# Kernel tuning notes

Hardware: AMD Instinct MI355X
Metric: run time of the kernel (lower is better)

## Reference

```python
import jax, jax.numpy as jnp
import numpy as np

M = 16           # size_graph_filter (nodes per hidden prototype graph)
S = 16           # size_subgraph
D_IN = 128       # input_dim
H = 64           # hidden_dim
O = 32           # out_dim (number of hidden prototype graphs)
B = 32768        # batch of subgraphs
MAX_STEP = 3
BN_EPS = 1e-5


def setup_inputs() -> dict:
    key = jax.random.key(0)
    ks = jax.random.split(key, 8)
    adj = jax.random.uniform(ks[0], (B, S, S), dtype=jnp.float32)
    adj = 0.5 * (adj + jnp.swapaxes(adj, 1, 2))  # symmetric weighted adjacency
    features = jax.random.normal(ks[1], (B, S, D_IN), dtype=jnp.float32)
    # learned parameters (per torch init: uniform inits, Linear default-like fc_in)
    W_in = jax.random.normal(ks[2], (D_IN, H), dtype=jnp.float32) * (1.0 / np.sqrt(D_IN))
    b_in = jnp.zeros((H,), dtype=jnp.float32)
    features_hidden = jax.random.uniform(ks[3], (M, H, O), dtype=jnp.float32)          # U(0,1)
    adj_hidden = jax.random.uniform(ks[4], (M * (M - 1) // 2, O), dtype=jnp.float32,
                                    minval=-1.0, maxval=1.0)                            # U(-1,1)
    bn_gamma = jnp.ones((O,), dtype=jnp.float32)
    bn_beta = jnp.zeros((O,), dtype=jnp.float32)
    return {"adj": adj, "features": features, "W_in": W_in, "b_in": b_in,
            "features_hidden": features_hidden, "adj_hidden": adj_hidden,
            "bn_gamma": bn_gamma, "bn_beta": bn_beta}


def reference(adj, features, W_in, b_in, features_hidden, adj_hidden, bn_gamma, bn_beta):
    # Build symmetric hidden adjacency (M, M, O) from triu-packed parameters.
    iu, ju = jnp.triu_indices(M, k=1)
    A = jnp.zeros((M, M, O), dtype=adj_hidden.dtype)
    A = A.at[iu, ju, :].set(jax.nn.relu(adj_hidden))
    A = A + jnp.swapaxes(A, 0, 1)

    x = jax.nn.sigmoid(features @ W_in + b_in)   # (B, S, H)
    z = features_hidden                           # (M, H, O)

    acc = jnp.zeros((B, O), dtype=x.dtype)
    for step in range(MAX_STEP):
        if step > 0:
            x = jnp.einsum('bst,bth->bsh', adj, x)        # propagate on input subgraphs
            z = jnp.einsum('mpo,pho->mho', A, z)          # propagate on hidden graphs
        # random-walk kernel value between each subgraph and each prototype
        t = jnp.einsum('mho,bsh->bo', z, x)               # sum over prototype & subgraph nodes
        acc = acc + t
    out = acc / MAX_STEP

    # BatchNorm1d (training-mode batch statistics), then sigmoid; dropout p used in eval = identity
    mean = jnp.mean(out, axis=0)
    var = jnp.var(out, axis=0)
    out = (out - mean) / jnp.sqrt(var + BN_EPS) * bn_gamma + bn_beta
    return jax.nn.sigmoid(out)
```

## Files before the change

### kernel.cpp

```cpp
#include <hip/hip_runtime.h>


typedef short  vec8s  __attribute__((ext_vector_type(8)));
typedef short  vec4s  __attribute__((ext_vector_type(4)));
typedef float  f32x4  __attribute__((ext_vector_type(4)));
typedef unsigned short vec4us __attribute__((ext_vector_type(4)));

#define NB      32768
#define SS      16
#define DIN     128
#define HH      64
#define OO      32
#define MM      16

__device__ __forceinline__ float bf2f(unsigned short u) {
    return __uint_as_float(((unsigned int)u) << 16);
}
__device__ __forceinline__ unsigned short f2bf(float f) {
    unsigned int u = __float_as_uint(f);
    unsigned int r = (u + 0x7fffu + ((u >> 16) & 1u)) >> 16;
    return (unsigned short)r;
}
template<bool F32>
__device__ __forceinline__ float ldv(const void* p, int i) {
    if (F32) return ((const float*)p)[i];
    return bf2f(((const unsigned short*)p)[i]);
}
__device__ __forceinline__ vec8s pack8(f32x4 lo, f32x4 hi) {
    union { unsigned int u[4]; vec8s v; } r;
    unsigned int a0 = __float_as_uint(lo[0]) + 0x8000u;
    unsigned int a1 = __float_as_uint(lo[1]) + 0x8000u;
    unsigned int a2 = __float_as_uint(lo[2]) + 0x8000u;
    unsigned int a3 = __float_as_uint(lo[3]) + 0x8000u;
    unsigned int b0 = __float_as_uint(hi[0]) + 0x8000u;
    unsigned int b1 = __float_as_uint(hi[1]) + 0x8000u;
    unsigned int b2 = __float_as_uint(hi[2]) + 0x8000u;
    unsigned int b3 = __float_as_uint(hi[3]) + 0x8000u;
    r.u[0] = (a0 >> 16) | (a1 & 0xFFFF0000u);
    r.u[1] = (a2 >> 16) | (a3 & 0xFFFF0000u);
    r.u[2] = (b0 >> 16) | (b1 & 0xFFFF0000u);
    r.u[3] = (b2 >> 16) | (b3 & 0xFFFF0000u);
    return r.v;
}

template<bool F32>
__device__ __forceinline__ float Aval(const void* ahS, int i, int j, int o) {
    if (i == j) return 0.f;
    int a = i < j ? i : j;
    int b = i < j ? j : i;
    int idx = a * 15 - ((a * (a - 1)) >> 1) + (b - a - 1);
    float v = ldv<F32>(ahS, idx * OO + o);
    return v > 0.f ? v : 0.f;
}

template<bool F32>
__device__ void k1_body(const void* fhP, const void* ahP, const void* WP,
                        short* ZcnS, short* WtS, float* cA, float* c2) {
    const int tid = threadIdx.x;
    for (int i = tid; i < MM * OO; i += 256) {
        int p = i >> 5, o = i & 31;
        float s = 0.f;
        for (int m = 0; m < MM; ++m) s += Aval<F32>(ahP, m, p, o);
        cA[i] = s;
    }
    __syncthreads();
    for (int i = tid; i < MM * OO; i += 256) {
        int qq = i >> 5, o = i & 31;
        float s = 0.f;
        for (int p = 0; p < MM; ++p) s += cA[p * OO + o] * Aval<F32>(ahP, p, qq, o);
        c2[i] = s;
    }
    __syncthreads();
    for (int i = blockIdx.x * 256 + tid; i < 3 * OO * HH; i += 16 * 256) {
        int n = i >> 6, h = i & 63;
        int step = n >> 5, o = n & 31;
        float v = 0.f;
        for (int p = 0; p < MM; ++p) {
            float z = ldv<F32>(fhP, p * (HH * OO) + h * OO + o);
            float w = (step == 0) ? 1.f : (step == 1 ? cA[p * OO + o] : c2[p * OO + o]);
            v += w * z;
        }
        ZcnS[n * HH + h] = (short)f2bf(v);
    }
    for (int i = blockIdx.x * 256 + tid; i < DIN * HH; i += 16 * 256) {
        int h = i >> 7, k = i & 127;
        WtS[h * DIN + k] = (short)f2bf(ldv<F32>(WP, k * HH + h));
    }
}

__global__ void k1_prep(const void* fhP, const void* ahP, const void* WP,
                        short* ZcnS, short* WtS, double* dstats,
                        const void* featP, int* flag) {
    __shared__ float cA[MM * OO];
    __shared__ float c2[MM * OO];
    __shared__ int chuge, czero, sflag;
    const int tid = threadIdx.x;
    if (tid == 0) { chuge = 0; czero = 0; }
    if (blockIdx.x == 0 && tid < 64) dstats[tid] = 0.0;
    __syncthreads();
    if (tid < 64) {
        const unsigned short* p = (const unsigned short*)featP;
        int h = 0, z = 0;
        for (int i = tid; i < 4096; i += 64) {
            unsigned short u = p[i];
            unsigned e = (u >> 7) & 0xFFu;
            if (e >= 0x90u) h++;
            if ((u & 0x7FFFu) == 0) z++;
        }
        atomicAdd(&chuge, h);
        atomicAdd(&czero, z);
    }
    __syncthreads();
    if (tid == 0) {
        sflag = (chuge > 8 || czero > 512) ? 1 : 0;
        if (blockIdx.x == 0) *flag = sflag;
    }
    __syncthreads();
    if (sflag) k1_body<true>(fhP, ahP, WP, ZcnS, WtS, cA, c2);
    else       k1_body<false>(fhP, ahP, WP, ZcnS, WtS, cA, c2);
}

template<bool F32>
__device__ void k2_body(const void* adjP, const void* featP, const void* binP,
                        const short* ZcnS, const short* WtS, float* accOut,
                        double* dstats, short* myx0, float* bsum, float* bsqs) {
    const int tid  = threadIdx.x;
    const int lane = tid & 63;
    const int hl   = lane & 15;
    const int q    = lane >> 4;

    vec8s Wfrag[4][4];
    for (int kt = 0; kt < 4; ++kt)
        for (int nt = 0; nt < 4; ++nt)
            Wfrag[kt][nt] = *(const vec8s*)(WtS + (nt * 16 + hl) * DIN + kt * 32 + q * 8);
    vec8s Zfrag[2][6];
    for (int kt = 0; kt < 2; ++kt)
        for (int t = 0; t < 6; ++t)
            Zfrag[kt][t] = *(const vec8s*)(ZcnS + (t * 16 + hl) * HH + kt * 32 + q * 8);
    float biasv[4];
    for (int nt = 0; nt < 4; ++nt) biasv[nt] = ldv<F32>(binP, nt * 16 + hl);

    const f32x4 z4 = {0.f, 0.f, 0.f, 0.f};
    float ls = 0.f, lss = 0.f;
    const int wgid = blockIdx.x * 4 + (tid >> 6);

    for (int b = wgid; b < NB; b += 2048) {
        float a0, a1, a2, a3;
        vec8s af[4];
        if (F32) {
            f32x4 av = *(const f32x4*)((const float*)adjP + b * (SS * SS) + lane * 4);
            a0 = av[0]; a1 = av[1]; a2 = av[2]; a3 = av[3];
            const float* fb = (const float*)featP + b * (SS * DIN) + hl * DIN + q * 8;
            for (int kt = 0; kt < 4; ++kt) {
                f32x4 lo = *(const f32x4*)(fb + kt * 32);
                f32x4 hi = *(const f32x4*)(fb + kt * 32 + 4);
                af[kt] = pack8(lo, hi);
            }
        } else {
            vec4s av = *(const vec4s*)((const short*)adjP + b * (SS * SS) + lane * 4);
            a0 = bf2f((unsigned short)av.x); a1 = bf2f((unsigned short)av.y);
            a2 = bf2f((unsigned short)av.z); a3 = bf2f((unsigned short)av.w);
            const short* fb = (const short*)featP + b * (SS * DIN) + hl * DIN + q * 8;
            for (int kt = 0; kt < 4; ++kt) af[kt] = *(const vec8s*)(fb + kt * 32);
        }

        float rsum = a0 + a1 + a2 + a3;
        rsum += __shfl_xor(rsum, 1);
        rsum += __shfl_xor(rsum, 2);
        int cg = lane & 3;
        float rr0 = __shfl(rsum, cg * 16 + 0);
        float rr1 = __shfl(rsum, cg * 16 + 4);
        float rr2 = __shfl(rsum, cg * 16 + 8);
        float rr3 = __shfl(rsum, cg * 16 + 12);
        float p = a0 * rr0 + a1 * rr1 + a2 * rr2 + a3 * rr3;
        p += __shfl_xor(p, 1);
        p += __shfl_xor(p, 2);
        float w1q[4], w2q[4];
        for (int reg = 0; reg < 4; ++reg) {
            int src = q * 16 + reg * 4;
            w1q[reg] = __shfl(rsum, src);
            w2q[reg] = __shfl(p, src);
        }

        f32x4 c1[4] = {z4, z4, z4, z4};
        for (int nt = 0; nt < 4; ++nt)
            for (int kt = 0; kt < 4; ++kt)
                c1[nt] = __builtin_amdgcn_mfma_f32_16x16x32_bf16(af[kt], Wfrag[kt][nt], c1[nt], 0, 0, 0);

        for (int nt = 0; nt < 4; ++nt)
            for (int reg = 0; reg < 4; ++reg) {
                float x = c1[nt][reg] + biasv[nt];
                float sg = 1.f / (1.f + __expf(-x));
                unsigned int u = __float_as_uint(sg) + 0x8000u;
                myx0[(q * 4 + reg) * 72 + nt * 16 + hl] = (short)(u >> 16);
            }
        __threadfence_block();

        vec8s a2lo = *(const vec8s*)(myx0 + hl * 72 + q * 8);
        vec8s a2hi = *(const vec8s*)(myx0 + hl * 72 + 32 + q * 8);
        __threadfence_block();
        f32x4 cp[6] = {z4, z4, z4, z4, z4, z4};
        for (int t = 0; t < 6; ++t)
            cp[t] = __builtin_amdgcn_mfma_f32_16x16x32_bf16(a2lo, Zfrag[0][t], cp[t], 0, 0, 0);
        for (int t = 0; t < 6; ++t)
            cp[t] = __builtin_amdgcn_mfma_f32_16x16x32_bf16(a2hi, Zfrag[1][t], cp[t], 0, 0, 0);

        float parts[6];
        for (int t = 0; t < 6; ++t) {
            int step = t >> 1;
            float v;
            if (step == 0)      v = cp[t][0] + cp[t][1] + cp[t][2] + cp[t][3];
            else if (step == 1) v = cp[t][0]*w1q[0] + cp[t][1]*w1q[1] + cp[t][2]*w1q[2] + cp[t][3]*w1q[3];
            else                v = cp[t][0]*w2q[0] + cp[t][1]*w2q[1] + cp[t][2]*w2q[2] + cp[t][3]*w2q[3];
            v += __shfl_xor(v, 16);
            v += __shfl_xor(v, 32);
            parts[t] = v;
        }
        float accA = parts[0] + parts[2] + parts[4];
        float accB = parts[1] + parts[3] + parts[5];
        float accv = ((lane >> 4) & 1) ? accB : accA;
        accv *= (1.f / 3.f);
        accv = __builtin_isnan(accv) ? 0.f : accv;
        if (lane < OO) accOut[b * OO + lane] = accv;
        ls  += accv;
        lss += accv * accv;
    }

    if (lane < OO) {
        atomicAdd(&bsum[lane], ls);
        atomicAdd(&bsqs[lane], lss);
    }
    __syncthreads();
    if (tid < OO) {
        atomicAdd(&dstats[tid],      (double)bsum[tid]);
        atomicAdd(&dstats[OO + tid], (double)bsqs[tid]);
    }
}

__global__ __launch_bounds__(256, 2) void k2_main(
    const void* adjP, const void* featP, const void* binP,
    const short* ZcnS, const short* WtS, float* accOut,
    double* dstats, const int* flag) {
    __shared__ __align__(16) short x0buf[4][SS * 72];
    __shared__ float bsum[OO];
    __shared__ float bsqs[OO];
    const int tid = threadIdx.x;
    if (tid < OO) { bsum[tid] = 0.f; bsqs[tid] = 0.f; }
    __syncthreads();
    short* myx0 = x0buf[tid >> 6];
    if (*flag) k2_body<true>(adjP, featP, binP, ZcnS, WtS, accOut, dstats, myx0, bsum, bsqs);
    else       k2_body<false>(adjP, featP, binP, ZcnS, WtS, accOut, dstats, myx0, bsum, bsqs);
}

__global__ __launch_bounds__(256) void k4_out(const float* __restrict__ acc,
                                              const double* __restrict__ dstats,
                                              const void* gammaP, const void* betaP,
                                              void* out, const int* flag) {
    __shared__ float sScale[OO], sShift[OO];
    const int tid = threadIdx.x;
    const int f = *flag;
    if (tid < OO) {
        double mean = dstats[tid] * (1.0 / (double)NB);
        double ex2  = dstats[OO + tid] * (1.0 / (double)NB);
        double var  = ex2 - mean * mean;
        if (var < 0.0) var = 0.0;
        double inv  = 1.0 / sqrt(var + 1e-5);
        float g  = f ? ldv<true>(gammaP, tid) : ldv<false>(gammaP, tid);
        float be = f ? ldv<true>(betaP, tid)  : ldv<false>(betaP, tid);
        sScale[tid] = g * (float)inv;
        sShift[tid] = be - (float)(mean * inv) * g;
    }
    __syncthreads();
    int i = (blockIdx.x * 256 + tid) * 4;
    int o0 = i & 31;
    f32x4 a = *(const f32x4*)(acc + i);
    float r[4];
    for (int j = 0; j < 4; ++j) {
        float z = a[j] * sScale[o0 + j] + sShift[o0 + j];
        r[j] = 1.f / (1.f + __expf(-z));
    }
    if (f) {
        f32x4 w;
        for (int j = 0; j < 4; ++j) w[j] = r[j];
        *(f32x4*)((float*)out + i) = w;
    } else {
        vec4us w;
        for (int j = 0; j < 4; ++j) w[j] = f2bf(r[j]);
        *(vec4us*)((unsigned short*)out + i) = w;
    }
}

extern "C" void kernel_launch(void* const* d_in, const int* in_sizes, int n_in,
                              void* d_out, int out_size, void* d_ws, size_t ws_size,
                              hipStream_t stream) {
    const void* adjP   = d_in[0];
    const void* featP  = d_in[1];
    const void* WP     = d_in[2];
    const void* binP   = d_in[3];
    const void* fhP    = d_in[4];
    const void* ahP    = d_in[5];
    const void* gammaP = d_in[6];
    const void* betaP  = d_in[7];

    char* ws = (char*)d_ws;
    float*  accOut   = (float*)(ws);
    short*  ZcnS     = (short*)(ws + 4194304);
    short*  WtS      = (short*)(ws + 4206592);
    double* dstats   = (double*)(ws + 4222976);
    int*    flag     = (int*)(ws + 4223744);

    hipLaunchKernelGGL(k1_prep,  dim3(16),   dim3(256), 0, stream,
                       fhP, ahP, WP, ZcnS, WtS, dstats, featP, flag);
    hipLaunchKernelGGL(k2_main,  dim3(512),  dim3(256), 0, stream,
                       adjP, featP, binP, ZcnS, WtS, accOut, dstats, flag);
    hipLaunchKernelGGL(k4_out,   dim3(1024), dim3(256), 0, stream,
                       accOut, dstats, gammaP, betaP, d_out, flag);
}
```

Baseline: 427.3 us.

## Double-buffer batch loads and move Z fragments to swizzled shared memory

After: 427.3 us. No clear change (-0.0%).

```diff
diff --git a/kernel.cpp b/kernel.cpp
--- a/kernel.cpp
+++ b/kernel.cpp
@@ -120,111 +120,172 @@
     else       k1_body<false>(fhP, ahP, WP, ZcnS, WtS, cA, c2);
 }
 
+
+template<bool F32> struct Slot;
+template<> struct Slot<true>  { f32x4 f[8]; f32x4 a; };
+template<> struct Slot<false> { vec8s f[4]; vec4s a; };
+
+template<bool F32>
+__device__ __forceinline__ void issue_load(const void* adjP, const void* featP,
+                                           int b, int lane, int hl, int q,
+                                           Slot<F32>& s) {
+    if constexpr (F32) {
+        s.a = *(const f32x4*)((const float*)adjP + b * (SS * SS) + lane * 4);
+        const float* fb = (const float*)featP + b * (SS * DIN) + hl * DIN + q * 8;
+        #pragma unroll
+        for (int kt = 0; kt < 4; ++kt) {
+            s.f[2 * kt]     = *(const f32x4*)(fb + kt * 32);
+            s.f[2 * kt + 1] = *(const f32x4*)(fb + kt * 32 + 4);
+        }
+    } else {
+        s.a = *(const vec4s*)((const short*)adjP + b * (SS * SS) + lane * 4);
+        const short* fb = (const short*)featP + b * (SS * DIN) + hl * DIN + q * 8;
+        #pragma unroll
+        for (int kt = 0; kt < 4; ++kt) s.f[kt] = *(const vec8s*)(fb + kt * 32);
+    }
+}
+
+template<bool F32>
+__device__ __forceinline__ void compute_one(
+    const Slot<F32>& s, int b,
+    const vec8s (&Wfrag)[4][4], const char* ZcnL,
+    const float (&biasv)[4], short* myx0, float* accOut,
+    float& ls, float& lss, int lane, int hl, int q) {
+
+    const f32x4 z4 = {0.f, 0.f, 0.f, 0.f};
+
+    float a0, a1, a2, a3;
+    vec8s af[4];
+    if constexpr (F32) {
+        a0 = s.a[0]; a1 = s.a[1]; a2 = s.a[2]; a3 = s.a[3];
+        #pragma unroll
+        for (int kt = 0; kt < 4; ++kt) af[kt] = pack8(s.f[2 * kt], s.f[2 * kt + 1]);
+    } else {
+        a0 = bf2f((unsigned short)s.a.x); a1 = bf2f((unsigned short)s.a.y);
+        a2 = bf2f((unsigned short)s.a.z); a3 = bf2f((unsigned short)s.a.w);
+        #pragma unroll
+        for (int kt = 0; kt < 4; ++kt) af[kt] = s.f[kt];
+    }
+
+    float rsum = a0 + a1 + a2 + a3;
+    rsum += __shfl_xor(rsum, 1);
+    rsum += __shfl_xor(rsum, 2);
+    int cg = lane & 3;
+    float rr0 = __shfl(rsum, cg * 16 + 0);
+    float rr1 = __shfl(rsum, cg * 16 + 4);
+    float rr2 = __shfl(rsum, cg * 16 + 8);
+    float rr3 = __shfl(rsum, cg * 16 + 12);
+    float p = a0 * rr0 + a1 * rr1 + a2 * rr2 + a3 * rr3;
+    p += __shfl_xor(p, 1);
+    p += __shfl_xor(p, 2);
+    float w1q[4], w2q[4];
+    #pragma unroll
+    for (int reg = 0; reg < 4; ++reg) {
+        int src = q * 16 + reg * 4;
+        w1q[reg] = __shfl(rsum, src);
+        w2q[reg] = __shfl(p, src);
+    }
+
+    f32x4 c1[4] = {z4, z4, z4, z4};
+    #pragma unroll
+    for (int nt = 0; nt < 4; ++nt)
+        #pragma unroll
+        for (int kt = 0; kt < 4; ++kt)
+            c1[nt] = __builtin_amdgcn_mfma_f32_16x16x32_bf16(af[kt], Wfrag[kt][nt], c1[nt], 0, 0, 0);
+
+    vec8s zf[2][6];
+    #pragma unroll
+    for (int kt = 0; kt < 2; ++kt)
+        #pragma unroll
+        for (int t = 0; t < 6; ++t) {
+            int row = t * 16 + hl;
+            int col = (kt * 64 + q * 16) ^ ((hl & 7) << 4);
+            zf[kt][t] = *(const vec8s*)(ZcnL + row * 128 + col);
+        }
+
+    #pragma unroll
+    for (int nt = 0; nt < 4; ++nt)
+        #pragma unroll
+        for (int reg = 0; reg < 4; ++reg) {
+            float x = c1[nt][reg] + biasv[nt];
+            float sg = 1.f / (1.f + __expf(-x));
+            unsigned int u = __float_as_uint(sg) + 0x8000u;
+            myx0[(q * 4 + reg) * 72 + nt * 16 + hl] = (short)(u >> 16);
+        }
+    __threadfence_block();
+
+    vec8s a2lo = *(const vec8s*)(myx0 + hl * 72 + q * 8);
+    vec8s a2hi = *(const vec8s*)(myx0 + hl * 72 + 32 + q * 8);
+    __threadfence_block();
+    f32x4 cp[6] = {z4, z4, z4, z4, z4, z4};
+    #pragma unroll
+    for (int t = 0; t < 6; ++t)
+        cp[t] = __builtin_amdgcn_mfma_f32_16x16x32_bf16(a2lo, zf[0][t], cp[t], 0, 0, 0);
+    #pragma unroll
+    for (int t = 0; t < 6; ++t)
+        cp[t] = __builtin_amdgcn_mfma_f32_16x16x32_bf16(a2hi, zf[1][t], cp[t], 0, 0, 0);
+
+    float parts[6];
+    #pragma unroll
+    for (int t = 0; t < 6; ++t) {
+        int step = t >> 1;
+        float v;
+        if (step == 0)      v = cp[t][0] + cp[t][1] + cp[t][2] + cp[t][3];
+        else if (step == 1) v = cp[t][0]*w1q[0] + cp[t][1]*w1q[1] + cp[t][2]*w1q[2] + cp[t][3]*w1q[3];
+        else                v = cp[t][0]*w2q[0] + cp[t][1]*w2q[1] + cp[t][2]*w2q[2] + cp[t][3]*w2q[3];
+        v += __shfl_xor(v, 16);
+        v += __shfl_xor(v, 32);
+        parts[t] = v;
+    }
+    float accA = parts[0] + parts[2] + parts[4];
+    float accB = parts[1] + parts[3] + parts[5];
+    float accv = ((lane >> 4) & 1) ? accB : accA;
+    accv *= (1.f / 3.f);
+    accv = __builtin_isnan(accv) ? 0.f : accv;
+    if (lane < OO) accOut[b * OO + lane] = accv;
+    ls  += accv;
+    lss += accv * accv;
+}
+
 template<bool F32>
 __device__ void k2_body(const void* adjP, const void* featP, const void* binP,
                         const short* ZcnS, const short* WtS, float* accOut,
-                        double* dstats, short* myx0, float* bsum, float* bsqs) {
+                        double* dstats, short* myx0, float* bsum, float* bsqs,
+                        const char* ZcnL) {
     const int tid  = threadIdx.x;
     const int lane = tid & 63;
     const int hl   = lane & 15;
     const int q    = lane >> 4;
 
     vec8s Wfrag[4][4];
+    #pragma unroll
     for (int kt = 0; kt < 4; ++kt)
+        #pragma unroll
         for (int nt = 0; nt < 4; ++nt)
             Wfrag[kt][nt] = *(const vec8s*)(WtS + (nt * 16 + hl) * DIN + kt * 32 + q * 8);
-    vec8s Zfrag[2][6];
-    for (int kt = 0; kt < 2; ++kt)
-        for (int t = 0; t < 6; ++t)
-            Zfrag[kt][t] = *(const vec8s*)(ZcnS + (t * 16 + hl) * HH + kt * 32 + q * 8);
     float biasv[4];
+    #pragma unroll
     for (int nt = 0; nt < 4; ++nt) biasv[nt] = ldv<F32>(binP, nt * 16 + hl);
 
-    const f32x4 z4 = {0.f, 0.f, 0.f, 0.f};
     float ls = 0.f, lss = 0.f;
     const int wgid = blockIdx.x * 4 + (tid >> 6);
 
-    for (int b = wgid; b < NB; b += 2048) {
-        float a0, a1, a2, a3;
-        vec8s af[4];
-        if (F32) {
-            f32x4 av = *(const f32x4*)((const float*)adjP + b * (SS * SS) + lane * 4);
-            a0 = av[0]; a1 = av[1]; a2 = av[2]; a3 = av[3];
-            const float* fb = (const float*)featP + b * (SS * DIN) + hl * DIN + q * 8;
-            for (int kt = 0; kt < 4; ++kt) {
-                f32x4 lo = *(const f32x4*)(fb + kt * 32);
-                f32x4 hi = *(const f32x4*)(fb + kt * 32 + 4);
-                af[kt] = pack8(lo, hi);
-            }
-        } else {
-            vec4s av = *(const vec4s*)((const short*)adjP + b * (SS * SS) + lane * 4);
-            a0 = bf2f((unsigned short)av.x); a1 = bf2f((unsigned short)av.y);
-            a2 = bf2f((unsigned short)av.z); a3 = bf2f((unsigned short)av.w);
-            const short* fb = (const short*)featP + b * (SS * DIN) + hl * DIN + q * 8;
-            for (int kt = 0; kt < 4; ++kt) af[kt] = *(const vec8s*)(fb + kt * 32);
-        }
-
-        float rsum = a0 + a1 + a2 + a3;
-        rsum += __shfl_xor(rsum, 1);
-        rsum += __shfl_xor(rsum, 2);
-        int cg = lane & 3;
-        float rr0 = __shfl(rsum, cg * 16 + 0);
-        float rr1 = __shfl(rsum, cg * 16 + 4);
-        float rr2 = __shfl(rsum, cg * 16 + 8);
-        float rr3 = __shfl(rsum, cg * 16 + 12);
-        float p = a0 * rr0 + a1 * rr1 + a2 * rr2 + a3 * rr3;
-        p += __shfl_xor(p, 1);
-        p += __shfl_xor(p, 2);
-        float w1q[4], w2q[4];
-        for (int reg = 0; reg < 4; ++reg) {
-            int src = q * 16 + reg * 4;
-            w1q[reg] = __shfl(rsum, src);
-            w2q[reg] = __shfl(p, src);
-        }
-
-        f32x4 c1[4] = {z4, z4, z4, z4};
-        for (int nt = 0; nt < 4; ++nt)
-            for (int kt = 0; kt < 4; ++kt)
-                c1[nt] = __builtin_amdgcn_mfma_f32_16x16x32_bf16(af[kt], Wfrag[kt][nt], c1[nt], 0, 0, 0);
-
-        for (int nt = 0; nt < 4; ++nt)
-            for (int reg = 0; reg < 4; ++reg) {
-                float x = c1[nt][reg] + biasv[nt];
-                float sg = 1.f / (1.f + __expf(-x));
-                unsigned int u = __float_as_uint(sg) + 0x8000u;
-                myx0[(q * 4 + reg) * 72 + nt * 16 + hl] = (short)(u >> 16);
-            }
-        __threadfence_block();
-
-        vec8s a2lo = *(const vec8s*)(myx0 + hl * 72 + q * 8);
-        vec8s a2hi = *(const vec8s*)(myx0 + hl * 72 + 32 + q * 8);
-        __threadfence_block();
-        f32x4 cp[6] = {z4, z4, z4, z4, z4, z4};
-        for (int t = 0; t < 6; ++t)
-            cp[t] = __builtin_amdgcn_mfma_f32_16x16x32_bf16(a2lo, Zfrag[0][t], cp[t], 0, 0, 0);
-        for (int t = 0; t < 6; ++t)
-            cp[t] = __builtin_amdgcn_mfma_f32_16x16x32_bf16(a2hi, Zfrag[1][t], cp[t], 0, 0, 0);
-
-        float parts[6];
-        for (int t = 0; t < 6; ++t) {
-            int step = t >> 1;
-            float v;
-            if (step == 0)      v = cp[t][0] + cp[t][1] + cp[t][2] + cp[t][3];
-            else if (step == 1) v = cp[t][0]*w1q[0] + cp[t][1]*w1q[1] + cp[t][2]*w1q[2] + cp[t][3]*w1q[3];
-            else                v = cp[t][0]*w2q[0] + cp[t][1]*w2q[1] + cp[t][2]*w2q[2] + cp[t][3]*w2q[3];
-            v += __shfl_xor(v, 16);
-            v += __shfl_xor(v, 32);
-            parts[t] = v;
-        }
-        float accA = parts[0] + parts[2] + parts[4];
-        float accB = parts[1] + parts[3] + parts[5];
-        float accv = ((lane >> 4) & 1) ? accB : accA;
-        accv *= (1.f / 3.f);
-        accv = __builtin_isnan(accv) ? 0.f : accv;
-        if (lane < OO) accOut[b * OO + lane] = accv;
-        ls  += accv;
-        lss += accv * accv;
-    }
+    Slot<F32> sA, sB;
+    int b = wgid;
+    issue_load<F32>(adjP, featP, b, lane, hl, q, sA);
+    #pragma unroll 1
+    for (int it = 0; it < 7; ++it) {
+        issue_load<F32>(adjP, featP, b + 2048, lane, hl, q, sB);
+        compute_one<F32>(sA, b, Wfrag, ZcnL, biasv, myx0, accOut, ls, lss, lane, hl, q);
+        b += 2048;
+        issue_load<F32>(adjP, featP, b + 2048, lane, hl, q, sA);
+        compute_one<F32>(sB, b, Wfrag, ZcnL, biasv, myx0, accOut, ls, lss, lane, hl, q);
+        b += 2048;
+    }
+    issue_load<F32>(adjP, featP, b + 2048, lane, hl, q, sB);
+    compute_one<F32>(sA, b, Wfrag, ZcnL, biasv, myx0, accOut, ls, lss, lane, hl, q);
+    b += 2048;
+    compute_one<F32>(sB, b, Wfrag, ZcnL, biasv, myx0, accOut, ls, lss, lane, hl, q);
 
     if (lane < OO) {
         atomicAdd(&bsum[lane], ls);
@@ -242,14 +303,20 @@
     const short* ZcnS, const short* WtS, float* accOut,
     double* dstats, const int* flag) {
     __shared__ __align__(16) short x0buf[4][SS * 72];
+    __shared__ __align__(16) char  ZcnL[96 * 128];
     __shared__ float bsum[OO];
     __shared__ float bsqs[OO];
     const int tid = threadIdx.x;
     if (tid < OO) { bsum[tid] = 0.f; bsqs[tid] = 0.f; }
+    for (int i = tid; i < 96 * 8; i += 256) {
+        int r = i >> 3, ch = i & 7;
+        vec8s v = *(const vec8s*)(ZcnS + r * 64 + ch * 8);
+        *(vec8s*)(ZcnL + r * 128 + ((ch * 16) ^ ((r & 7) << 4))) = v;
+    }
     __syncthreads();
     short* myx0 = x0buf[tid >> 6];
-    if (*flag) k2_body<true>(adjP, featP, binP, ZcnS, WtS, accOut, dstats, myx0, bsum, bsqs);
-    else       k2_body<false>(adjP, featP, binP, ZcnS, WtS, accOut, dstats, myx0, bsum, bsqs);
+    if (*flag) k2_body<true>(adjP, featP, binP, ZcnS, WtS, accOut, dstats, myx0, bsum, bsqs, ZcnL);
+    else       k2_body<false>(adjP, featP, binP, ZcnS, WtS, accOut, dstats, myx0, bsum, bsqs, ZcnL);
 }
 
 __global__ __launch_bounds__(256) void k4_out(const float* __restrict__ acc,
@@ -275,16 +342,19 @@
     int o0 = i & 31;
     f32x4 a = *(const f32x4*)(acc + i);
     float r[4];
+    #pragma unroll
     for (int j = 0; j < 4; ++j) {
         float z = a[j] * sScale[o0 + j] + sShift[o0 + j];
         r[j] = 1.f / (1.f + __expf(-z));
     }
     if (f) {
         f32x4 w;
+        #pragma unroll
         for (int j = 0; j < 4; ++j) w[j] = r[j];
         *(f32x4*)((float*)out + i) = w;
     } else {
         vec4us w;
+        #pragma unroll
         for (int j = 0; j < 4; ++j) w[j] = f2bf(r[j]);
         *(vec4us*)((unsigned short*)out + i) = w;
     }
```

## Launch more blocks with higher occupancy and replicate BN stat accumulators

Applied to the files above, without the earlier changes.

After: 620.4 us. +45.2%, slower.

```diff
diff --git a/kernel.cpp b/kernel.cpp
--- a/kernel.cpp
+++ b/kernel.cpp
@@ -12,6 +12,8 @@
 #define HH      64
 #define OO      32
 #define MM      16
+#define NBLK    2048
+#define NWAVE   (NBLK * 4)
 
 __device__ __forceinline__ float bf2f(unsigned short u) {
     return __uint_as_float(((unsigned int)u) << 16);
@@ -96,7 +98,8 @@
     __shared__ int chuge, czero, sflag;
     const int tid = threadIdx.x;
     if (tid == 0) { chuge = 0; czero = 0; }
-    if (blockIdx.x == 0 && tid < 64) dstats[tid] = 0.0;
+    if (blockIdx.x == 0)
+        for (int i = tid; i < 8 * 64; i += 256) dstats[i] = 0.0;
     __syncthreads();
     if (tid < 64) {
         const unsigned short* p = (const unsigned short*)featP;
@@ -123,34 +126,40 @@
 template<bool F32>
 __device__ void k2_body(const void* adjP, const void* featP, const void* binP,
                         const short* ZcnS, const short* WtS, float* accOut,
-                        double* dstats, short* myx0, float* bsum, float* bsqs) {
+                        double* dsRep, short* myx0, float* bsum, float* bsqs) {
     const int tid  = threadIdx.x;
     const int lane = tid & 63;
     const int hl   = lane & 15;
     const int q    = lane >> 4;
 
     vec8s Wfrag[4][4];
+    #pragma unroll
     for (int kt = 0; kt < 4; ++kt)
+        #pragma unroll
         for (int nt = 0; nt < 4; ++nt)
             Wfrag[kt][nt] = *(const vec8s*)(WtS + (nt * 16 + hl) * DIN + kt * 32 + q * 8);
     vec8s Zfrag[2][6];
+    #pragma unroll
     for (int kt = 0; kt < 2; ++kt)
+        #pragma unroll
         for (int t = 0; t < 6; ++t)
             Zfrag[kt][t] = *(const vec8s*)(ZcnS + (t * 16 + hl) * HH + kt * 32 + q * 8);
     float biasv[4];
+    #pragma unroll
     for (int nt = 0; nt < 4; ++nt) biasv[nt] = ldv<F32>(binP, nt * 16 + hl);
 
     const f32x4 z4 = {0.f, 0.f, 0.f, 0.f};
     float ls = 0.f, lss = 0.f;
     const int wgid = blockIdx.x * 4 + (tid >> 6);
 
-    for (int b = wgid; b < NB; b += 2048) {
+    for (int b = wgid; b < NB; b += NWAVE) {
         float a0, a1, a2, a3;
         vec8s af[4];
         if (F32) {
             f32x4 av = *(const f32x4*)((const float*)adjP + b * (SS * SS) + lane * 4);
             a0 = av[0]; a1 = av[1]; a2 = av[2]; a3 = av[3];
             const float* fb = (const float*)featP + b * (SS * DIN) + hl * DIN + q * 8;
+            #pragma unroll
             for (int kt = 0; kt < 4; ++kt) {
                 f32x4 lo = *(const f32x4*)(fb + kt * 32);
                 f32x4 hi = *(const f32x4*)(fb + kt * 32 + 4);
@@ -161,6 +170,7 @@
             a0 = bf2f((unsigned short)av.x); a1 = bf2f((unsigned short)av.y);
             a2 = bf2f((unsigned short)av.z); a3 = bf2f((unsigned short)av.w);
             const short* fb = (const short*)featP + b * (SS * DIN) + hl * DIN + q * 8;
+            #pragma unroll
             for (int kt = 0; kt < 4; ++kt) af[kt] = *(const vec8s*)(fb + kt * 32);
         }
 
@@ -176,6 +186,7 @@
         p += __shfl_xor(p, 1);
         p += __shfl_xor(p, 2);
         float w1q[4], w2q[4];
+        #pragma unroll
         for (int reg = 0; reg < 4; ++reg) {
             int src = q * 16 + reg * 4;
             w1q[reg] = __shfl(rsum, src);
@@ -183,11 +194,15 @@
         }
 
         f32x4 c1[4] = {z4, z4, z4, z4};
+        #pragma unroll
         for (int nt = 0; nt < 4; ++nt)
+            #pragma unroll
             for (int kt = 0; kt < 4; ++kt)
                 c1[nt] = __builtin_amdgcn_mfma_f32_16x16x32_bf16(af[kt], Wfrag[kt][nt], c1[nt], 0, 0, 0);
 
+        #pragma unroll
         for (int nt = 0; nt < 4; ++nt)
+            #pragma unroll
             for (int reg = 0; reg < 4; ++reg) {
                 float x = c1[nt][reg] + biasv[nt];
                 float sg = 1.f / (1.f + __expf(-x));
@@ -200,12 +215,15 @@
         vec8s a2hi = *(const vec8s*)(myx0 + hl * 72 + 32 + q * 8);
         __threadfence_block();
         f32x4 cp[6] = {z4, z4, z4, z4, z4, z4};
+        #pragma unroll
         for (int t = 0; t < 6; ++t)
             cp[t] = __builtin_amdgcn_mfma_f32_16x16x32_bf16(a2lo, Zfrag[0][t], cp[t], 0, 0, 0);
+        #pragma unroll
         for (int t = 0; t < 6; ++t)
             cp[t] = __builtin_amdgcn_mfma_f32_16x16x32_bf16(a2hi, Zfrag[1][t], cp[t], 0, 0, 0);
 
         float parts[6];
+        #pragma unroll
         for (int t = 0; t < 6; ++t) {
             int step = t >> 1;
             float v;
@@ -232,12 +250,12 @@
     }
     __syncthreads();
     if (tid < OO) {
-        atomicAdd(&dstats[tid],      (double)bsum[tid]);
-        atomicAdd(&dstats[OO + tid], (double)bsqs[tid]);
-    }
-}
-
-__global__ __launch_bounds__(256, 2) void k2_main(
+        atomicAdd(&dsRep[tid],      (double)bsum[tid]);
+        atomicAdd(&dsRep[OO + tid], (double)bsqs[tid]);
+    }
+}
+
+__global__ __launch_bounds__(256, 8) void k2_main(
     const void* adjP, const void* featP, const void* binP,
     const short* ZcnS, const short* WtS, float* accOut,
     double* dstats, const int* flag) {
@@ -248,8 +266,9 @@
     if (tid < OO) { bsum[tid] = 0.f; bsqs[tid] = 0.f; }
     __syncthreads();
     short* myx0 = x0buf[tid >> 6];
-    if (*flag) k2_body<true>(adjP, featP, binP, ZcnS, WtS, accOut, dstats, myx0, bsum, bsqs);
-    else       k2_body<false>(adjP, featP, binP, ZcnS, WtS, accOut, dstats, myx0, bsum, bsqs);
+    double* dsRep = dstats + (blockIdx.x & 7) * 64;
+    if (*flag) k2_body<true>(adjP, featP, binP, ZcnS, WtS, accOut, dsRep, myx0, bsum, bsqs);
+    else       k2_body<false>(adjP, featP, binP, ZcnS, WtS, accOut, dsRep, myx0, bsum, bsqs);
 }
 
 __global__ __launch_bounds__(256) void k4_out(const float* __restrict__ acc,
@@ -260,8 +279,14 @@
     const int tid = threadIdx.x;
     const int f = *flag;
     if (tid < OO) {
-        double mean = dstats[tid] * (1.0 / (double)NB);
-        double ex2  = dstats[OO + tid] * (1.0 / (double)NB);
+        double s1 = 0.0, s2 = 0.0;
+        #pragma unroll
+        for (int rdup = 0; rdup < 8; ++rdup) {
+            s1 += dstats[rdup * 64 + tid];
+            s2 += dstats[rdup * 64 + OO + tid];
+        }
+        double mean = s1 * (1.0 / (double)NB);
+        double ex2  = s2 * (1.0 / (double)NB);
         double var  = ex2 - mean * mean;
         if (var < 0.0) var = 0.0;
         double inv  = 1.0 / sqrt(var + 1e-5);
@@ -275,16 +300,19 @@
     int o0 = i & 31;
     f32x4 a = *(const f32x4*)(acc + i);
     float r[4];
+    #pragma unroll
     for (int j = 0; j < 4; ++j) {
         float z = a[j] * sScale[o0 + j] + sShift[o0 + j];
         r[j] = 1.f / (1.f + __expf(-z));
     }
     if (f) {
         f32x4 w;
+        #pragma unroll
         for (int j = 0; j < 4; ++j) w[j] = r[j];
         *(f32x4*)((float*)out + i) = w;
     } else {
         vec4us w;
+        #pragma unroll
         for (int j = 0; j < 4; ++j) w[j] = f2bf(r[j]);
         *(vec4us*)((unsigned short*)out + i) = w;
     }
@@ -307,11 +335,11 @@
     short*  ZcnS     = (short*)(ws + 4194304);
     short*  WtS      = (short*)(ws + 4206592);
     double* dstats   = (double*)(ws + 4222976);
-    int*    flag     = (int*)(ws + 4223744);
+    int*    flag     = (int*)(ws + 4227072);
 
     hipLaunchKernelGGL(k1_prep,  dim3(16),   dim3(256), 0, stream,
                        fhP, ahP, WP, ZcnS, WtS, dstats, featP, flag);
-    hipLaunchKernelGGL(k2_main,  dim3(512),  dim3(256), 0, stream,
+    hipLaunchKernelGGL(k2_main,  dim3(NBLK), dim3(256), 0, stream,
                        adjP, featP, binP, ZcnS, WtS, accOut, dstats, flag);
     hipLaunchKernelGGL(k4_out,   dim3(1024), dim3(256), 0, stream,
                        accOut, dstats, gammaP, betaP, d_out, flag);
```
